# Kernel optimization log

Hardware: AMD Instinct MI355X
Metric: run time of the kernel (lower is better)

The kernel has to match this reference:

```python
import jax, jax.numpy as jnp
import numpy as np

D_MODEL = 2048
D_HEAD = 64
Q_HEADS = 32
KV_HEADS = 8


def rope(x):
    # x: [B, S, H, D], rotate interleaved pairs along last dim
    B, S, H, D = x.shape
    pos = jnp.arange(S, dtype=x.dtype)
    freq = 1.0 / (10000.0 ** (jnp.arange(0, D, 2, dtype=x.dtype) / D))  # [D/2]
    theta = pos[:, None] * freq[None, :]                                 # [S, D/2]
    cos = jnp.cos(theta)[None, :, None, :]
    sin = jnp.sin(theta)[None, :, None, :]
    xr = x.reshape(B, S, H, D // 2, 2)
    x1, x2 = xr[..., 0], xr[..., 1]
    out = jnp.stack((x1 * cos - x2 * sin, x1 * sin + x2 * cos), axis=-1)
    return out.reshape(B, S, H, D)


def setup_inputs() -> dict:
    key = jax.random.key(0)
    ks = jax.random.split(key, 7)
    x = jax.random.normal(ks[0], (1, 2048, D_MODEL), dtype=jnp.float32)
    W_q = jax.random.normal(ks[1], (Q_HEADS * D_HEAD, D_MODEL), dtype=jnp.float32) * 0.02
    b_q = jnp.zeros((Q_HEADS * D_HEAD,), dtype=jnp.float32)
    W_kv = jax.random.normal(ks[2], (2 * KV_HEADS * D_HEAD, D_MODEL), dtype=jnp.float32) * 0.02
    b_kv = jnp.zeros((2 * KV_HEADS * D_HEAD,), dtype=jnp.float32)
    W_out = jax.random.normal(ks[3], (D_MODEL, D_MODEL), dtype=jnp.float32) * 0.02
    b_out = jnp.zeros((D_MODEL,), dtype=jnp.float32)
    return {"x": x, "W_q": W_q, "b_q": b_q, "W_kv": W_kv, "b_kv": b_kv,
            "W_out": W_out, "b_out": b_out}


def reference(x, W_q, b_q, W_kv, b_kv, W_out, b_out):
    B, S, _ = x.shape
    g = Q_HEADS // KV_HEADS
    Q = (x @ W_q.T + b_q).reshape(B, S, Q_HEADS, D_HEAD)
    kv = x @ W_kv.T + b_kv
    K, V = jnp.split(kv, 2, axis=-1)
    K = K.reshape(B, S, KV_HEADS, D_HEAD)
    V = V.reshape(B, S, KV_HEADS, D_HEAD)
    Q = rope(Q)
    K = rope(K)
    K = jnp.repeat(K, g, axis=2)  # [B, S, Q_HEADS, D_HEAD]
    V = jnp.repeat(V, g, axis=2)
    scale = 1.0 / (D_HEAD ** 0.5)
    scores = jnp.einsum('bqhd,bkhd->bhqk', Q, K) * scale  # [B,H,S,S]
    # note: original calls non-inplace masked_fill and discards it, so no causal mask applied
    probs = jax.nn.softmax(scores, axis=-1)
    attn = jnp.einsum('bhqk,bkhd->bqhd', probs, V).reshape(B, S, D_MODEL)
    return attn @ W_out.T + b_out
```

## Files before the change

kernel.cpp:

```cpp
#include <hip/hip_runtime.h>
#include <hip/hip_bf16.h>
#include <math.h>

#define S_LEN 2048
#define D_MODEL 2048
#define Q_HEADS 32
#define KV_HEADS 8

typedef __attribute__((ext_vector_type(8))) short short8;
typedef __attribute__((ext_vector_type(4))) float f32x4;

__device__ __forceinline__ short bf16_rne(float f) {
  unsigned u = __float_as_uint(f);
  unsigned r = (u + 0x7FFFu + ((u >> 16) & 1u)) >> 16;
  return (short)r;
}
__device__ __forceinline__ void dma16(const short* g, short* l) {
  __builtin_amdgcn_global_load_lds(
      (const __attribute__((address_space(1))) void*)g,
      (__attribute__((address_space(3))) void*)l, 16, 0, 0);
}
__device__ __forceinline__ void fast_sincos(float theta, float& sn, float& cs) {
  double rev = (double)theta * 0.15915494309189535;
  float fr = (float)(rev - floor(rev));
  sn = __builtin_amdgcn_sinf(fr);
  cs = __builtin_amdgcn_cosf(fr);
}
__device__ __forceinline__ void cvt8(const float* src, short* dst, int i) {
  float4 a = *(const float4*)&src[i];
  float4 b = *(const float4*)&src[i + 4];
  short8 h;
  h[0] = bf16_rne(a.x); h[1] = bf16_rne(a.y);
  h[2] = bf16_rne(a.z); h[3] = bf16_rne(a.w);
  h[4] = bf16_rne(b.x); h[5] = bf16_rne(b.y);
  h[6] = bf16_rne(b.z); h[7] = bf16_rne(b.w);
  *(short8*)&dst[i] = h;
}

#define NM (2048 * 2048)
#define NKV (1024 * 2048)

__global__ __launch_bounds__(256) void cvt_all(
    const float* __restrict__ x,    short* __restrict__ xh,
    const float* __restrict__ wq,   short* __restrict__ wqh,
    const float* __restrict__ wkv,  short* __restrict__ wkvh,
    const float* __restrict__ wo,   short* __restrict__ woh) {
  int i = (blockIdx.x * 256 + threadIdx.x) * 8;
  if (i < NM) { cvt8(x, xh, i); return; }
  i -= NM;
  if (i < NM) { cvt8(wq, wqh, i); return; }
  i -= NM;
  if (i < NKV) { cvt8(wkv, wkvh, i); return; }
  i -= NKV;
  cvt8(wo, woh, i);
}

__global__ __launch_bounds__(256) void gemm_nt1_dual(
    const short* __restrict__ Ah,
    const short* __restrict__ Bq, const short* __restrict__ Bkv,
    const float* __restrict__ bq, const float* __restrict__ bkv,
    float* __restrict__ Cq, float* __restrict__ Ckv,
    int Nq, int Nkv, int K) {
  __shared__ short As[2][128 * 32];
  __shared__ short Bs[2][128 * 32];
  const int tid = threadIdx.x;
  const int w = tid >> 6, lane = tid & 63;
  const int l16 = lane & 15, quad = lane >> 4;
  const int bm = blockIdx.y * 128;
  const int bnG = blockIdx.x * 128;

  const short* Bsrc; const float* bias; float* Cp; int pitch; int bn;
  if (bnG < Nq) { Bsrc = Bq;  bias = bq;  Cp = Cq;  pitch = Nq;  bn = bnG; }
  else          { Bsrc = Bkv; bias = bkv; Cp = Ckv; pitch = Nkv; bn = bnG - Nq; }

  const int drow0 = w * 16 + (lane >> 2);
  const int drow1 = drow0 + 64;
  const int slot = lane & 3;
  const int ch0 = slot ^ ((drow0 >> 1) & 3);
  const int ch1 = slot ^ ((drow1 >> 1) & 3);
  const short* gA0 = &Ah[(size_t)(bm + drow0) * K + ch0 * 8];
  const short* gA1 = &Ah[(size_t)(bm + drow1) * K + ch1 * 8];
  const short* gB0 = &Bsrc[(size_t)(bn + drow0) * K + ch0 * 8];
  const short* gB1 = &Bsrc[(size_t)(bn + drow1) * K + ch1 * 8];
  const int dA0 = (w * 16) * 32, dA1 = (64 + w * 16) * 32;

  const int wm = (w & 1) * 64, wn = (w >> 1) * 64;
  int offA[4], offB[4];
#pragma unroll
  for (int i = 0; i < 4; ++i) {
    int R = wm + i * 16 + l16;
    offA[i] = R * 32 + (quad ^ ((R >> 1) & 3)) * 8;
    int Rb = wn + i * 16 + l16;
    offB[i] = Rb * 32 + (quad ^ ((Rb >> 1) & 3)) * 8;
  }

  f32x4 acc[4][4];
#pragma unroll
  for (int i = 0; i < 4; ++i)
#pragma unroll
    for (int j = 0; j < 4; ++j)
#pragma unroll
      for (int e = 0; e < 4; ++e) acc[i][j][e] = 0.f;

  const int T = K / 32;
  dma16(gA0, &As[0][dA0]);
  dma16(gA1, &As[0][dA1]);
  dma16(gB0, &Bs[0][dA0]);
  dma16(gB1, &Bs[0][dA1]);
  __syncthreads();

  for (int t = 0; t < T; ++t) {
    const int cur = t & 1, nxt = cur ^ 1;
    if (t + 1 < T) {
      const int ko = (t + 1) * 32;
      dma16(gA0 + ko, &As[nxt][dA0]);
      dma16(gA1 + ko, &As[nxt][dA1]);
      dma16(gB0 + ko, &Bs[nxt][dA0]);
      dma16(gB1 + ko, &Bs[nxt][dA1]);
    }
    short8 af[4], bf[4];
#pragma unroll
    for (int i = 0; i < 4; ++i) af[i] = *(const short8*)&As[cur][offA[i]];
#pragma unroll
    for (int j = 0; j < 4; ++j) bf[j] = *(const short8*)&Bs[cur][offB[j]];
#pragma unroll
    for (int i = 0; i < 4; ++i)
#pragma unroll
      for (int j = 0; j < 4; ++j)
        acc[i][j] = __builtin_amdgcn_mfma_f32_16x16x32_bf16(af[i], bf[j], acc[i][j], 0, 0, 0);
    __syncthreads();
  }

#pragma unroll
  for (int i = 0; i < 4; ++i) {
#pragma unroll
    for (int j = 0; j < 4; ++j) {
      const int col = bn + wn + j * 16 + l16;
      const float bv = bias[col];
      const int row0 = bm + wm + i * 16 + quad * 4;
#pragma unroll
      for (int e = 0; e < 4; ++e)
        Cp[(size_t)(row0 + e) * pitch + col] = acc[i][j][e] + bv;
    }
  }
}

__global__ __launch_bounds__(256) void gemm_nt1_big(
    const short* __restrict__ A, const short* __restrict__ B,
    const float* __restrict__ bias, float* __restrict__ C,
    int N, int K) {
  __shared__ short As[2][128 * 32];
  __shared__ short Bs[2][128 * 32];
  const int tid = threadIdx.x;
  const int w = tid >> 6, lane = tid & 63;
  const int l16 = lane & 15, quad = lane >> 4;
  const int bm = blockIdx.y * 128;
  const int bn = blockIdx.x * 128;

  const int drow0 = w * 16 + (lane >> 2);
  const int drow1 = drow0 + 64;
  const int slot = lane & 3;
  const int ch0 = slot ^ ((drow0 >> 1) & 3);
  const int ch1 = slot ^ ((drow1 >> 1) & 3);
  const short* gA0 = &A[(size_t)(bm + drow0) * K + ch0 * 8];
  const short* gA1 = &A[(size_t)(bm + drow1) * K + ch1 * 8];
  const short* gB0 = &B[(size_t)(bn + drow0) * K + ch0 * 8];
  const short* gB1 = &B[(size_t)(bn + drow1) * K + ch1 * 8];
  const int dA0 = (w * 16) * 32, dA1 = (64 + w * 16) * 32;

  const int wm = (w & 1) * 64, wn = (w >> 1) * 64;
  int offA[4], offB[4];
#pragma unroll
  for (int i = 0; i < 4; ++i) {
    int R = wm + i * 16 + l16;
    offA[i] = R * 32 + (quad ^ ((R >> 1) & 3)) * 8;
    int Rb = wn + i * 16 + l16;
    offB[i] = Rb * 32 + (quad ^ ((Rb >> 1) & 3)) * 8;
  }

  f32x4 acc[4][4];
#pragma unroll
  for (int i = 0; i < 4; ++i)
#pragma unroll
    for (int j = 0; j < 4; ++j)
#pragma unroll
      for (int e = 0; e < 4; ++e) acc[i][j][e] = 0.f;

  const int T = K / 32;
  dma16(gA0, &As[0][dA0]);
  dma16(gA1, &As[0][dA1]);
  dma16(gB0, &Bs[0][dA0]);
  dma16(gB1, &Bs[0][dA1]);
  __syncthreads();

  for (int t = 0; t < T; ++t) {
    const int cur = t & 1, nxt = cur ^ 1;
    if (t + 1 < T) {
      const int ko = (t + 1) * 32;
      dma16(gA0 + ko, &As[nxt][dA0]);
      dma16(gA1 + ko, &As[nxt][dA1]);
      dma16(gB0 + ko, &Bs[nxt][dA0]);
      dma16(gB1 + ko, &Bs[nxt][dA1]);
    }
    short8 af[4], bf[4];
#pragma unroll
    for (int i = 0; i < 4; ++i) af[i] = *(const short8*)&As[cur][offA[i]];
#pragma unroll
    for (int j = 0; j < 4; ++j) bf[j] = *(const short8*)&Bs[cur][offB[j]];
#pragma unroll
    for (int i = 0; i < 4; ++i)
#pragma unroll
      for (int j = 0; j < 4; ++j)
        acc[i][j] = __builtin_amdgcn_mfma_f32_16x16x32_bf16(af[i], bf[j], acc[i][j], 0, 0, 0);
    __syncthreads();
  }

#pragma unroll
  for (int i = 0; i < 4; ++i) {
#pragma unroll
    for (int j = 0; j < 4; ++j) {
      const int col = bn + wn + j * 16 + l16;
      const float bv = bias[col];
      const int row0 = bm + wm + i * 16 + quad * 4;
#pragma unroll
      for (int e = 0; e < 4; ++e)
        C[(size_t)(row0 + e) * N + col] = acc[i][j][e] + bv;
    }
  }
}

#define QSCALE 0.18033688011112042f

__global__ __launch_bounds__(256) void rope_q_pack(
    const float* __restrict__ Qf, short* __restrict__ Qb) {
  const int g = blockIdx.x * 256 + threadIdx.x;
  const int s = g >> 10;
  const int rem = g & 1023;
  const int h = rem >> 5, j = rem & 31;
  const double e = (2.0 * j) / 64.0;
  const float freq = (float)pow(10000.0, -e);
  const float theta = (float)s * freq;
  float sn, cs;
  fast_sincos(theta, sn, cs);
  const float* p = &Qf[(size_t)s * D_MODEL + h * 64 + 2 * j];
  const float x1 = p[0], x2 = p[1];
  short2 o;
  o.x = bf16_rne((x1 * cs - x2 * sn) * QSCALE);
  o.y = bf16_rne((x1 * sn + x2 * cs) * QSCALE);
  *(short2*)&Qb[((size_t)h * S_LEN + s) * 64 + 2 * j] = o;
}

__global__ __launch_bounds__(256) void rope_kv_pack(
    const float* __restrict__ KVf, short* __restrict__ Kb,
    short* __restrict__ Vt) {
  const int st = blockIdx.x, kvh = blockIdx.y;
  const int tid = threadIdx.x;
  __shared__ short Vtile[64][72];

  {
    const int sr = tid >> 2, sc = (tid & 3) * 16;
    const int s = st * 64 + sr;
    const float* kg = &KVf[(size_t)s * 1024 + kvh * 64 + sc];
    short tmp[16];
#pragma unroll
    for (int i = 0; i < 8; ++i) {
      const int j = (sc >> 1) + i;
      const double e = (2.0 * j) / 64.0;
      const float freq = (float)pow(10000.0, -e);
      const float theta = (float)s * freq;
      float sn, cs;
      fast_sincos(theta, sn, cs);
      const float x1 = kg[2 * i], x2 = kg[2 * i + 1];
      tmp[2 * i]     = bf16_rne(x1 * cs - x2 * sn);
      tmp[2 * i + 1] = bf16_rne(x1 * sn + x2 * cs);
    }
    short* out = &Kb[((size_t)kvh * S_LEN + s) * 64 + sc];
    *(short8*)&out[0] = *(short8*)&tmp[0];
    *(short8*)&out[8] = *(short8*)&tmp[8];
  }

  {
    const int sr = tid >> 2, sc = (tid & 3) * 16;
    const float* vg = &KVf[(size_t)(st * 64 + sr) * 1024 + 512 + kvh * 64 + sc];
    short tmp[16];
#pragma unroll
    for (int c = 0; c < 16; c += 4) {
      float4 v = *(const float4*)&vg[c];
      tmp[c + 0] = bf16_rne(v.x);
      tmp[c + 1] = bf16_rne(v.y);
      tmp[c + 2] = bf16_rne(v.z);
      tmp[c + 3] = bf16_rne(v.w);
    }
    *(short8*)&Vtile[sr][sc]     = *(short8*)&tmp[0];
    *(short8*)&Vtile[sr][sc + 8] = *(short8*)&tmp[8];
  }
  __syncthreads();
  {
    const int d = tid & 63, kchunk = tid >> 6;
    short tmp[16];
#pragma unroll
    for (int k = 0; k < 16; ++k) tmp[k] = Vtile[kchunk * 16 + k][d];
    short* out = &Vt[((size_t)kvh * 64 + d) * S_LEN + st * 64 + kchunk * 16];
    *(short8*)&out[0] = *(short8*)&tmp[0];
    *(short8*)&out[8] = *(short8*)&tmp[8];
  }
}

__global__ __launch_bounds__(256, 4) void flash8(
    const short* __restrict__ Qb, const short* __restrict__ Kb,
    const short* __restrict__ Vt, short* __restrict__ Oh) {
  const int qt = blockIdx.x, h = blockIdx.y;
  const int kvh = h >> 2;
  const int tid = threadIdx.x;
  const int w = tid >> 6, lane = tid & 63;
  const int l16 = lane & 15, quad = lane >> 4;

  __shared__ short Ks[2][64 * 64];
  __shared__ short Vs[2][64 * 64];
  __shared__ short Ps[64 * 64];

  const short* Kh = Kb + (size_t)kvh * S_LEN * 64;
  const short* Vh = Vt + (size_t)kvh * 64 * S_LEN;
  const int qr = qt * 64 + w * 16 + l16;

  short8 qf0 = *(const short8*)&Qb[((size_t)h * S_LEN + qr) * 64 + quad * 8];
  short8 qf1 = *(const short8*)&Qb[((size_t)h * S_LEN + qr) * 64 + 32 + quad * 8];

  short8 ones;
#pragma unroll
  for (int e = 0; e < 8; ++e) ones[e] = (short)0x3F80;

  const int drow = lane >> 3;
  const int ch = (lane & 7) ^ drow;
  const short* gK = &Kh[(size_t)(w * 16 + drow) * 64 + ch * 8];
  const short* gV = &Vh[(size_t)(w * 16 + drow) * S_LEN + ch * 8];

  const int sl0 = quad ^ (l16 & 7);
  int offT[4][2];
#pragma unroll
  for (int m = 0; m < 4; ++m) {
    offT[m][0] = (m * 16 + l16) * 64 + sl0 * 8;
    offT[m][1] = (m * 16 + l16) * 64 + (sl0 ^ 4) * 8;
  }

  const int prow = (w * 16 + l16) * 64;
  const int pswz = (l16 & 7) << 1;
  int pwr[4];
#pragma unroll
  for (int m = 0; m < 4; ++m) pwr[m] = prow + ((4 * m + quad) ^ pswz) * 4;
  const int prd0 = prow + ((2 * quad) ^ pswz) * 4;
  const int prd1 = prow + ((8 + 2 * quad) ^ pswz) * 4;

  f32x4 accl;
#pragma unroll
  for (int e = 0; e < 4; ++e) accl[e] = 0.f;
  f32x4 acco[4];
#pragma unroll
  for (int m = 0; m < 4; ++m)
#pragma unroll
    for (int e = 0; e < 4; ++e) acco[m][e] = 0.f;

  dma16(gK,               &Ks[0][(w * 16) * 64]);
  dma16(gK + 8 * 64,      &Ks[0][(w * 16 + 8) * 64]);
  dma16(gV,               &Vs[0][(w * 16) * 64]);
  dma16(gV + 8 * S_LEN,   &Vs[0][(w * 16 + 8) * 64]);
  __syncthreads();

  for (int t = 0; t < 32; ++t) {
    const int cur = t & 1, nxt = cur ^ 1;
    if (t + 1 < 32) {
      const short* gKn = gK + (t + 1) * 4096;
      const short* gVn = gV + (t + 1) * 64;
      dma16(gKn,             &Ks[nxt][(w * 16) * 64]);
      dma16(gKn + 8 * 64,    &Ks[nxt][(w * 16 + 8) * 64]);
      dma16(gVn,             &Vs[nxt][(w * 16) * 64]);
      dma16(gVn + 8 * S_LEN, &Vs[nxt][(w * 16 + 8) * 64]);
    }

    const short* kc = Ks[cur];
    f32x4 accs[4];
#pragma unroll
    for (int m = 0; m < 4; ++m)
#pragma unroll
      for (int e = 0; e < 4; ++e) accs[m][e] = 0.f;
#pragma unroll
    for (int m = 0; m < 4; ++m) {
      short8 k0 = *(const short8*)&kc[offT[m][0]];
      short8 k1 = *(const short8*)&kc[offT[m][1]];
      accs[m] = __builtin_amdgcn_mfma_f32_16x16x32_bf16(k0, qf0, accs[m], 0, 0, 0);
      accs[m] = __builtin_amdgcn_mfma_f32_16x16x32_bf16(k1, qf1, accs[m], 0, 0, 0);
    }

#pragma unroll
    for (int m = 0; m < 4; ++m) {
      float p0 = exp2f(accs[m][0]);
      float p1 = exp2f(accs[m][1]);
      float p2 = exp2f(accs[m][2]);
      float p3 = exp2f(accs[m][3]);
      unsigned u01 = __builtin_amdgcn_perm(__float_as_uint(p1), __float_as_uint(p0), 0x07060302u);
      unsigned u23 = __builtin_amdgcn_perm(__float_as_uint(p3), __float_as_uint(p2), 0x07060302u);
      *(uint2*)&Ps[pwr[m]] = make_uint2(u01, u23);
    }

    short8 pf0 = *(const short8*)&Ps[prd0];
    short8 pf1 = *(const short8*)&Ps[prd1];
    accl = __builtin_amdgcn_mfma_f32_16x16x32_bf16(ones, pf0, accl, 0, 0, 0);
    accl = __builtin_amdgcn_mfma_f32_16x16x32_bf16(ones, pf1, accl, 0, 0, 0);
    const short* vc = Vs[cur];
#pragma unroll
    for (int m = 0; m < 4; ++m) {
      short8 v0 = *(const short8*)&vc[offT[m][0]];
      short8 v1 = *(const short8*)&vc[offT[m][1]];
      acco[m] = __builtin_amdgcn_mfma_f32_16x16x32_bf16(v0, pf0, acco[m], 0, 0, 0);
      acco[m] = __builtin_amdgcn_mfma_f32_16x16x32_bf16(v1, pf1, acco[m], 0, 0, 0);
    }

    __syncthreads();
  }

  const float inv = 1.f / accl[0];
#pragma unroll
  for (int m = 0; m < 4; ++m) {
    short4 h4;
    h4.x = bf16_rne(acco[m][0] * inv);
    h4.y = bf16_rne(acco[m][1] * inv);
    h4.z = bf16_rne(acco[m][2] * inv);
    h4.w = bf16_rne(acco[m][3] * inv);
    const size_t base = (size_t)qr * D_MODEL + h * 64 + m * 16 + quad * 4;
    *(short4*)&Oh[base] = h4;
  }
}

extern "C" void kernel_launch(void* const* d_in, const int* in_sizes, int n_in,
                              void* d_out, int out_size, void* d_ws, size_t ws_size,
                              hipStream_t stream) {
  const float* x     = (const float*)d_in[0];
  const float* W_q   = (const float*)d_in[1];
  const float* b_q   = (const float*)d_in[2];
  const float* W_kv  = (const float*)d_in[3];
  const float* b_kv  = (const float*)d_in[4];
  const float* W_out = (const float*)d_in[5];
  const float* b_out = (const float*)d_in[6];
  float* out = (float*)d_out;

  char* ws = (char*)d_ws;
  float* Qbuf  = (float*)(ws);
  float* KVbuf = (float*)(ws + (16u << 20));
  short* xh    = (short*)(ws + (24u << 20));
  short* Wqh   = (short*)(ws + (32u << 20));
  short* Wkvh  = (short*)(ws + (40u << 20));
  short* Woh   = (short*)(ws + (44u << 20));
  short* Qb    = (short*)(ws + (52u << 20));
  short* Kb    = (short*)(ws + (60u << 20));
  short* Vtb   = (short*)(ws + (62u << 20));
  short* Ath   = xh;

  cvt_all<<<7168, 256, 0, stream>>>(x, xh, W_q, Wqh, W_kv, Wkvh, W_out, Woh);

  gemm_nt1_dual<<<dim3(3072 / 128, 2048 / 128), 256, 0, stream>>>(
      xh, Wqh, Wkvh, b_q, b_kv, Qbuf, KVbuf, 2048, 1024, 2048);

  rope_q_pack<<<(S_LEN * 1024) / 256, 256, 0, stream>>>(Qbuf, Qb);
  rope_kv_pack<<<dim3(S_LEN / 64, KV_HEADS), 256, 0, stream>>>(KVbuf, Kb, Vtb);

  flash8<<<dim3(S_LEN / 64, Q_HEADS), 256, 0, stream>>>(Qb, Kb, Vtb, Ath);

  gemm_nt1_big<<<dim3(2048 / 128, 2048 / 128), 256, 0, stream>>>(
      Ath, Woh, b_out, out, 2048, 2048);
}
```

Measured before the change: 268.3 us.

## Shrink QKV GEMM N-tile, precompute RoPE freq table, merge RoPE kernels

The fused QKV projection GEMM now uses 128x64 tiles instead of 128x128, doubling the block count from 384 to 768 so more of the GPU's compute units are occupied. The double-precision pow per element in the RoPE kernels is replaced by a 32-entry frequency table written once by the conversion kernel. The separate Q and KV RoPE kernels are merged into one launch to save launch overhead. The smaller tile lowers per-block data reuse, so global and LDS traffic per FLOP rises.

```diff
diff --git a/kernel.cpp b/kernel.cpp
--- a/kernel.cpp
+++ b/kernel.cpp
@@ -44,7 +44,12 @@
     const float* __restrict__ x,    short* __restrict__ xh,
     const float* __restrict__ wq,   short* __restrict__ wqh,
     const float* __restrict__ wkv,  short* __restrict__ wkvh,
-    const float* __restrict__ wo,   short* __restrict__ woh) {
+    const float* __restrict__ wo,   short* __restrict__ woh,
+    float* __restrict__ freqTab) {
+  if (blockIdx.x == 0 && threadIdx.x < 32) {
+    const double e = (2.0 * threadIdx.x) / 64.0;
+    freqTab[threadIdx.x] = (float)pow(10000.0, -e);
+  }
   int i = (blockIdx.x * 256 + threadIdx.x) * 8;
   if (i < NM) { cvt8(x, xh, i); return; }
   i -= NM;
@@ -62,12 +67,12 @@
     float* __restrict__ Cq, float* __restrict__ Ckv,
     int Nq, int Nkv, int K) {
   __shared__ short As[2][128 * 32];
-  __shared__ short Bs[2][128 * 32];
+  __shared__ short Bs[2][64 * 32];
   const int tid = threadIdx.x;
   const int w = tid >> 6, lane = tid & 63;
   const int l16 = lane & 15, quad = lane >> 4;
   const int bm = blockIdx.y * 128;
-  const int bnG = blockIdx.x * 128;
+  const int bnG = blockIdx.x * 64;
 
   const short* Bsrc; const float* bias; float* Cp; int pitch; int bn;
   if (bnG < Nq) { Bsrc = Bq;  bias = bq;  Cp = Cq;  pitch = Nq;  bn = bnG; }
@@ -78,55 +83,55 @@
   const int slot = lane & 3;
   const int ch0 = slot ^ ((drow0 >> 1) & 3);
   const int ch1 = slot ^ ((drow1 >> 1) & 3);
-  const short* gA0 = &Ah[(size_t)(bm + drow0) * K + ch0 * 8];
-  const short* gA1 = &Ah[(size_t)(bm + drow1) * K + ch1 * 8];
-  const short* gB0 = &Bsrc[(size_t)(bn + drow0) * K + ch0 * 8];
-  const short* gB1 = &Bsrc[(size_t)(bn + drow1) * K + ch1 * 8];
+  const size_t a0 = (size_t)(bm + drow0) * K + ch0 * 8;
+  const size_t a1 = (size_t)(bm + drow1) * K + ch1 * 8;
+  const size_t b0 = (size_t)(bn + drow0) * K + ch0 * 8;
   const int dA0 = (w * 16) * 32, dA1 = (64 + w * 16) * 32;
 
-  const int wm = (w & 1) * 64, wn = (w >> 1) * 64;
-  int offA[4], offB[4];
+  const int wm = (w & 1) * 64, wn = (w >> 1) * 32;
+  int offA[4], offB[2];
 #pragma unroll
   for (int i = 0; i < 4; ++i) {
     int R = wm + i * 16 + l16;
     offA[i] = R * 32 + (quad ^ ((R >> 1) & 3)) * 8;
-    int Rb = wn + i * 16 + l16;
-    offB[i] = Rb * 32 + (quad ^ ((Rb >> 1) & 3)) * 8;
-  }
-
-  f32x4 acc[4][4];
+  }
+#pragma unroll
+  for (int j = 0; j < 2; ++j) {
+    int R = wn + j * 16 + l16;
+    offB[j] = R * 32 + (quad ^ ((R >> 1) & 3)) * 8;
+  }
+
+  f32x4 acc[4][2];
 #pragma unroll
   for (int i = 0; i < 4; ++i)
 #pragma unroll
-    for (int j = 0; j < 4; ++j)
+    for (int j = 0; j < 2; ++j)
 #pragma unroll
       for (int e = 0; e < 4; ++e) acc[i][j][e] = 0.f;
 
   const int T = K / 32;
-  dma16(gA0, &As[0][dA0]);
-  dma16(gA1, &As[0][dA1]);
-  dma16(gB0, &Bs[0][dA0]);
-  dma16(gB1, &Bs[0][dA1]);
+  dma16(Ah + a0, &As[0][dA0]);
+  dma16(Ah + a1, &As[0][dA1]);
+  dma16(Bsrc + b0, &Bs[0][dA0]);
   __syncthreads();
 
   for (int t = 0; t < T; ++t) {
     const int cur = t & 1, nxt = cur ^ 1;
     if (t + 1 < T) {
       const int ko = (t + 1) * 32;
-      dma16(gA0 + ko, &As[nxt][dA0]);
-      dma16(gA1 + ko, &As[nxt][dA1]);
-      dma16(gB0 + ko, &Bs[nxt][dA0]);
-      dma16(gB1 + ko, &Bs[nxt][dA1]);
-    }
-    short8 af[4], bf[4];
+      dma16(Ah + a0 + ko, &As[nxt][dA0]);
+      dma16(Ah + a1 + ko, &As[nxt][dA1]);
+      dma16(Bsrc + b0 + ko, &Bs[nxt][dA0]);
+    }
+    short8 af[4], bf[2];
 #pragma unroll
     for (int i = 0; i < 4; ++i) af[i] = *(const short8*)&As[cur][offA[i]];
 #pragma unroll
-    for (int j = 0; j < 4; ++j) bf[j] = *(const short8*)&Bs[cur][offB[j]];
+    for (int j = 0; j < 2; ++j) bf[j] = *(const short8*)&Bs[cur][offB[j]];
 #pragma unroll
     for (int i = 0; i < 4; ++i)
 #pragma unroll
-      for (int j = 0; j < 4; ++j)
+      for (int j = 0; j < 2; ++j)
         acc[i][j] = __builtin_amdgcn_mfma_f32_16x16x32_bf16(af[i], bf[j], acc[i][j], 0, 0, 0);
     __syncthreads();
   }
@@ -134,7 +139,7 @@
 #pragma unroll
   for (int i = 0; i < 4; ++i) {
 #pragma unroll
-    for (int j = 0; j < 4; ++j) {
+    for (int j = 0; j < 2; ++j) {
       const int col = bn + wn + j * 16 + l16;
       const float bv = bias[col];
       const int row0 = bm + wm + i * 16 + quad * 4;
@@ -231,31 +236,32 @@
 
 #define QSCALE 0.18033688011112042f
 
-__global__ __launch_bounds__(256) void rope_q_pack(
-    const float* __restrict__ Qf, short* __restrict__ Qb) {
-  const int g = blockIdx.x * 256 + threadIdx.x;
-  const int s = g >> 10;
-  const int rem = g & 1023;
-  const int h = rem >> 5, j = rem & 31;
-  const double e = (2.0 * j) / 64.0;
-  const float freq = (float)pow(10000.0, -e);
-  const float theta = (float)s * freq;
-  float sn, cs;
-  fast_sincos(theta, sn, cs);
-  const float* p = &Qf[(size_t)s * D_MODEL + h * 64 + 2 * j];
-  const float x1 = p[0], x2 = p[1];
-  short2 o;
-  o.x = bf16_rne((x1 * cs - x2 * sn) * QSCALE);
-  o.y = bf16_rne((x1 * sn + x2 * cs) * QSCALE);
-  *(short2*)&Qb[((size_t)h * S_LEN + s) * 64 + 2 * j] = o;
-}
-
-__global__ __launch_bounds__(256) void rope_kv_pack(
-    const float* __restrict__ KVf, short* __restrict__ Kb,
-    short* __restrict__ Vt) {
-  const int st = blockIdx.x, kvh = blockIdx.y;
+__global__ __launch_bounds__(256) void rope_all(
+    const float* __restrict__ Qf, const float* __restrict__ KVf,
+    const float* __restrict__ tab, short* __restrict__ Qb,
+    short* __restrict__ Kb, short* __restrict__ Vt) {
+  __shared__ short Vtile[64][72];
   const int tid = threadIdx.x;
-  __shared__ short Vtile[64][72];
+
+  if (blockIdx.x < 8192) {
+    const int g = blockIdx.x * 256 + tid;
+    const int s = g >> 10;
+    const int rem = g & 1023;
+    const int h = rem >> 5, j = rem & 31;
+    const float theta = (float)s * tab[j];
+    float sn, cs;
+    fast_sincos(theta, sn, cs);
+    const float* p = &Qf[(size_t)s * D_MODEL + h * 64 + 2 * j];
+    const float x1 = p[0], x2 = p[1];
+    short2 o;
+    o.x = bf16_rne((x1 * cs - x2 * sn) * QSCALE);
+    o.y = bf16_rne((x1 * sn + x2 * cs) * QSCALE);
+    *(short2*)&Qb[((size_t)h * S_LEN + s) * 64 + 2 * j] = o;
+    return;
+  }
+
+  const int bb = blockIdx.x - 8192;
+  const int st = bb & 31, kvh = bb >> 5;
 
   {
     const int sr = tid >> 2, sc = (tid & 3) * 16;
@@ -265,9 +271,7 @@
 #pragma unroll
     for (int i = 0; i < 8; ++i) {
       const int j = (sc >> 1) + i;
-      const double e = (2.0 * j) / 64.0;
-      const float freq = (float)pow(10000.0, -e);
-      const float theta = (float)s * freq;
+      const float theta = (float)s * tab[j];
       float sn, cs;
       fast_sincos(theta, sn, cs);
       const float x1 = kg[2 * i], x2 = kg[2 * i + 1];
@@ -453,15 +457,16 @@
   short* Qb    = (short*)(ws + (52u << 20));
   short* Kb    = (short*)(ws + (60u << 20));
   short* Vtb   = (short*)(ws + (62u << 20));
+  float* freqTab = (float*)(ws + (64u << 20));
   short* Ath   = xh;
 
-  cvt_all<<<7168, 256, 0, stream>>>(x, xh, W_q, Wqh, W_kv, Wkvh, W_out, Woh);
-
-  gemm_nt1_dual<<<dim3(3072 / 128, 2048 / 128), 256, 0, stream>>>(
+  cvt_all<<<7168, 256, 0, stream>>>(x, xh, W_q, Wqh, W_kv, Wkvh, W_out, Woh,
+                                    freqTab);
+
+  gemm_nt1_dual<<<dim3(3072 / 64, 2048 / 128), 256, 0, stream>>>(
       xh, Wqh, Wkvh, b_q, b_kv, Qbuf, KVbuf, 2048, 1024, 2048);
 
-  rope_q_pack<<<(S_LEN * 1024) / 256, 256, 0, stream>>>(Qbuf, Qb);
-  rope_kv_pack<<<dim3(S_LEN / 64, KV_HEADS), 256, 0, stream>>>(KVbuf, Kb, Vtb);
+  rope_all<<<8192 + 256, 256, 0, stream>>>(Qbuf, KVbuf, freqTab, Qb, Kb, Vtb);
 
   flash8<<<dim3(S_LEN / 64, Q_HEADS), 256, 0, stream>>>(Qb, Kb, Vtb, Ath);
 
```

After: 264.2 us. No clear change (-1.5%).
